# Performance work log

Measured on AMD Instinct MI355X. Metric: run time of the kernel, lower is better.

Reference implementation:

```python
import jax, jax.numpy as jnp
import numpy as np

FFT_N = 320.0  # one-sided 161-bin spectrum of a 320-point FFT


def setup_inputs() -> dict:
    key = jax.random.key(0)
    spec = jax.random.normal(key, (32, 4000, 161, 2), dtype=jnp.float32)
    return {"spec": spec}


def _frame_gain(spec):
    # spec: [B, T, F, 2] -> per-frame RMS gain g0: [B, T]
    spec_pow = jnp.sum(spec * spec, axis=-1)  # [B, T, F]
    p = (jnp.sum(spec_pow[..., 1:-1], axis=-1) * 2.0
         + spec_pow[..., 0] + spec_pow[..., -1]) / FFT_N  # [B, T]
    return jnp.sqrt(p)


def _ema_over_time(g0):
    # g[0] = g0[0]; g[n] = 0.9*g[n-1] + 0.1*g0[n]  (scan over time axis 1)
    def step(carry, x):
        c = carry * 0.9 + x * 0.1
        return c, c
    init = g0[:, 0]                       # [B]
    xs = jnp.swapaxes(g0[:, 1:], 0, 1)    # [T-1, B]
    _, outs = jax.lax.scan(step, init, xs)  # [T-1, B]
    return jnp.concatenate([g0[:, :1], jnp.swapaxes(outs, 0, 1)], axis=1)  # [B, T]


def reference(spec):
    g0 = _frame_gain(spec)                        # [B, T]
    gain = _ema_over_time(g0)[:, :, None, None]   # [B, T, 1, 1]
    new_spec = spec / (gain + 0.001)              # [B, T, F, 2]
    return new_spec, gain
```

## Files before the change

kernel.cpp:

```cpp
#include <hip/hip_runtime.h>


typedef float f32x4 __attribute__((ext_vector_type(4)));
typedef float f32x2 __attribute__((ext_vector_type(2)));

#define B_SZ 32
#define T_SZ 4000
#define FRAME_F 322
#define FRAMES (B_SZ * T_SZ)
#define N_SPEC ((size_t)FRAMES * FRAME_F)
#define EMA_W 384
#define HALO (EMA_W - 1)
#define BLOCK 256
#define NGROUPS (FRAMES / 2)
#define CHUNK 250
#define NCHUNK (T_SZ / CHUNK)
#define C4 (CHUNK * FRAME_F / 4)
#define XS_N (HALO + CHUNK)

__global__ __launch_bounds__(BLOCK) void k_frame_gain(
    const float* __restrict__ spec, float* __restrict__ g0) {
  int grp = (blockIdx.x * BLOCK + threadIdx.x) >> 3;
  int sub = threadIdx.x & 7;
  if (grp >= NGROUPS) return;

  const float* base = spec + (size_t)grp * 644;
  float accA = 0.f, accB = 0.f;
  float pw0A = 0.f, pw160A = 0.f, pw0B = 0.f, pw160B = 0.f;

#pragma unroll
  for (int k = 0; k < 21; ++k) {
    int idx = k * 8 + sub;
    if (idx < 161) {
      f32x4 v = *(const f32x4*)(base + idx * 4);
      float s01 = v.x * v.x + v.y * v.y;
      float s23 = v.z * v.z + v.w * v.w;
      if (idx < 80) {
        accA += s01 + s23;
        if (idx == 0) pw0A = s01;
      } else if (idx == 80) {
        accA += s01; accB += s23;
        pw160A = s01;
        pw0B   = s23;
      } else {
        accB += s01 + s23;
        if (idx == 160) pw160B = s23;
      }
    }
  }
#pragma unroll
  for (int off = 1; off < 8; off <<= 1) {
    accA += __shfl_xor(accA, off, 64);
    accB += __shfl_xor(accB, off, 64);
  }
  if (sub == 0) {
    f32x2 g;
    g.x = sqrtf((2.f * accA - pw0A - pw160A) * (1.0f / 320.0f));
    g.y = sqrtf((2.f * accB - pw0B - pw160B) * (1.0f / 320.0f));
    *(f32x2*)(g0 + 2 * grp) = g;
  }
}

__global__ __launch_bounds__(BLOCK) void k_ema_apply(
    const float* __restrict__ spec, const float* __restrict__ g0,
    float* __restrict__ out, float* __restrict__ gain_out) {
  __shared__ float xs[XS_N];
  __shared__ float inv_s[CHUNK];

  int c  = blockIdx.x;
  int b  = blockIdx.y;
  int t0 = c * CHUNK;
  int lo = t0 - HALO; if (lo < 0) lo = 0;
  int n  = t0 + CHUNK - lo;
  int tid = threadIdx.x;
  const float* gb = g0 + b * T_SZ;

  for (int i = tid; i < n; i += BLOCK) xs[i] = gb[lo + i];
  __syncthreads();

  if (tid < CHUNK) {
    int t = t0 + tid;
    int s = t - HALO; if (s < 1) s = 1;
    float cc = (s == 1) ? xs[0] : 0.f;
    for (int k = s; k <= t; ++k) cc = cc * 0.9f + xs[k - lo] * 0.1f;
    gain_out[b * T_SZ + t] = cc;
    inv_s[tid] = 1.0f / (cc + 0.001f);
  }
  __syncthreads();

  size_t base4 = ((size_t)b * T_SZ + t0) * FRAME_F / 4;
  const f32x4* sp = (const f32x4*)spec + base4;
  f32x4*       op = (f32x4*)out  + base4;
#pragma unroll 8
  for (int i = tid; i < C4; i += BLOCK) {
    f32x4 v = sp[i];
    unsigned p0 = (unsigned)(2 * i);
    unsigned lf = p0 / 161u;
    unsigned r  = p0 - lf * 161u;
    unsigned lf1 = lf + (r == 160u);
    float i0 = inv_s[lf];
    float i1 = inv_s[lf1];
    f32x4 rr;
    rr.x = v.x * i0; rr.y = v.y * i0;
    rr.z = v.z * i1; rr.w = v.w * i1;
    __builtin_nontemporal_store(rr, op + i);
  }
}

extern "C" void kernel_launch(void* const* d_in, const int* in_sizes, int n_in,
                              void* d_out, int out_size, void* d_ws, size_t ws_size,
                              hipStream_t stream) {
  const float* spec = (const float*)d_in[0];
  float* out  = (float*)d_out;
  float* gain = out + N_SPEC;
  float* g0   = (float*)d_ws;

  k_frame_gain<<<NGROUPS * 8 / BLOCK, BLOCK, 0, stream>>>(spec, g0);

  dim3 g23(NCHUNK, B_SZ);
  k_ema_apply<<<g23, BLOCK, 0, stream>>>(spec, g0, out, gain);
}
```

Baseline: 95.39 us.

## Fuse frame-gain and EMA-apply into one kernel with inter-block flag sync

```diff
diff --git a/kernel.cpp b/kernel.cpp
--- a/kernel.cpp
+++ b/kernel.cpp
@@ -11,59 +11,17 @@
 #define N_SPEC ((size_t)FRAMES * FRAME_F)
 #define EMA_W 384
 #define HALO (EMA_W - 1)
-#define BLOCK 256
-#define NGROUPS (FRAMES / 2)
-#define CHUNK 250
+#define BLOCK 512
+#define CHUNK 200
 #define NCHUNK (T_SZ / CHUNK)
+#define GRPS (CHUNK / 2)
 #define C4 (CHUNK * FRAME_F / 4)
 #define XS_N (HALO + CHUNK)
 
-__global__ __launch_bounds__(BLOCK) void k_frame_gain(
-    const float* __restrict__ spec, float* __restrict__ g0) {
-  int grp = (blockIdx.x * BLOCK + threadIdx.x) >> 3;
-  int sub = threadIdx.x & 7;
-  if (grp >= NGROUPS) return;
-
-  const float* base = spec + (size_t)grp * 644;
-  float accA = 0.f, accB = 0.f;
-  float pw0A = 0.f, pw160A = 0.f, pw0B = 0.f, pw160B = 0.f;
-
-#pragma unroll
-  for (int k = 0; k < 21; ++k) {
-    int idx = k * 8 + sub;
-    if (idx < 161) {
-      f32x4 v = *(const f32x4*)(base + idx * 4);
-      float s01 = v.x * v.x + v.y * v.y;
-      float s23 = v.z * v.z + v.w * v.w;
-      if (idx < 80) {
-        accA += s01 + s23;
-        if (idx == 0) pw0A = s01;
-      } else if (idx == 80) {
-        accA += s01; accB += s23;
-        pw160A = s01;
-        pw0B   = s23;
-      } else {
-        accB += s01 + s23;
-        if (idx == 160) pw160B = s23;
-      }
-    }
-  }
-#pragma unroll
-  for (int off = 1; off < 8; off <<= 1) {
-    accA += __shfl_xor(accA, off, 64);
-    accB += __shfl_xor(accB, off, 64);
-  }
-  if (sub == 0) {
-    f32x2 g;
-    g.x = sqrtf((2.f * accA - pw0A - pw160A) * (1.0f / 320.0f));
-    g.y = sqrtf((2.f * accB - pw0B - pw160B) * (1.0f / 320.0f));
-    *(f32x2*)(g0 + 2 * grp) = g;
-  }
-}
-
-__global__ __launch_bounds__(BLOCK) void k_ema_apply(
-    const float* __restrict__ spec, const float* __restrict__ g0,
-    float* __restrict__ out, float* __restrict__ gain_out) {
+__global__ __launch_bounds__(BLOCK) void k_flow(
+    const float* __restrict__ spec, float* __restrict__ out,
+    float* __restrict__ gain_out, float* __restrict__ g0,
+    int* __restrict__ flags) {
   __shared__ float xs[XS_N];
   __shared__ float inv_s[CHUNK];
 
@@ -71,11 +29,63 @@
   int b  = blockIdx.y;
   int t0 = c * CHUNK;
   int lo = t0 - HALO; if (lo < 0) lo = 0;
-  int n  = t0 + CHUNK - lo;
+  int hn = t0 - lo;
   int tid = threadIdx.x;
-  const float* gb = g0 + b * T_SZ;
+  int sub = tid & 7;
 
-  for (int i = tid; i < n; i += BLOCK) xs[i] = gb[lo + i];
+  const float* srow = spec + (size_t)b * T_SZ * FRAME_F;
+  float* grow = g0 + b * T_SZ;
+
+  for (int gl = tid >> 3; gl < GRPS; gl += BLOCK / 8) {
+    const float* base = srow + (size_t)(t0 + 2 * gl) * FRAME_F;
+    float accA = 0.f, accB = 0.f;
+    float pw0A = 0.f, pw160A = 0.f, pw0B = 0.f, pw160B = 0.f;
+#pragma unroll
+    for (int k = 0; k < 21; ++k) {
+      int idx = k * 8 + sub;
+      if (idx < 161) {
+        f32x4 v = *(const f32x4*)(base + idx * 4);
+        float s01 = v.x * v.x + v.y * v.y;
+        float s23 = v.z * v.z + v.w * v.w;
+        if (idx < 80) {
+          accA += s01 + s23;
+          if (idx == 0) pw0A = s01;
+        } else if (idx == 80) {
+          accA += s01; accB += s23;
+          pw160A = s01;
+          pw0B   = s23;
+        } else {
+          accB += s01 + s23;
+          if (idx == 160) pw160B = s23;
+        }
+      }
+    }
+#pragma unroll
+    for (int off = 1; off < 8; off <<= 1) {
+      accA += __shfl_xor(accA, off, 64);
+      accB += __shfl_xor(accB, off, 64);
+    }
+    if (sub == 0) {
+      float gA = sqrtf((2.f * accA - pw0A - pw160A) * (1.0f / 320.0f));
+      float gB = sqrtf((2.f * accB - pw0B - pw160B) * (1.0f / 320.0f));
+      xs[hn + 2 * gl]     = gA;
+      xs[hn + 2 * gl + 1] = gB;
+      f32x2 g; g.x = gA; g.y = gB;
+      *(f32x2*)(grow + t0 + 2 * gl) = g;
+    }
+  }
+  __syncthreads();
+
+  if (tid == 0) {
+    __threadfence();
+    atomicExch(&flags[b * NCHUNK + c], 1);
+    for (int p = c - 1; p >= 0 && p >= c - 2; --p)
+      while (atomicAdd(&flags[b * NCHUNK + p], 0) == 0) {}
+    __threadfence();
+  }
+  __syncthreads();
+
+  for (int i = tid; i < hn; i += BLOCK) xs[i] = grow[lo + i];
   __syncthreads();
 
   if (tid < CHUNK) {
@@ -91,7 +101,7 @@
   size_t base4 = ((size_t)b * T_SZ + t0) * FRAME_F / 4;
   const f32x4* sp = (const f32x4*)spec + base4;
   f32x4*       op = (f32x4*)out  + base4;
-#pragma unroll 8
+#pragma unroll 4
   for (int i = tid; i < C4; i += BLOCK) {
     f32x4 v = sp[i];
     unsigned p0 = (unsigned)(2 * i);
@@ -114,9 +124,10 @@
   float* out  = (float*)d_out;
   float* gain = out + N_SPEC;
   float* g0   = (float*)d_ws;
+  int*   flags = (int*)(g0 + FRAMES);
 
-  k_frame_gain<<<NGROUPS * 8 / BLOCK, BLOCK, 0, stream>>>(spec, g0);
+  hipMemsetAsync(flags, 0, B_SZ * NCHUNK * sizeof(int), stream);
 
-  dim3 g23(NCHUNK, B_SZ);
-  k_ema_apply<<<g23, BLOCK, 0, stream>>>(spec, g0, out, gain);
+  dim3 grid(NCHUNK, B_SZ);
+  k_flow<<<grid, BLOCK, 0, stream>>>(spec, out, gain, g0, flags);
 }
```

After: 125.7 us. 1.32x slower.
